# Performance work log

Measured on AMD Instinct MI355X. Metric: run time of the kernel, lower is better.

## Reference

```python
import jax, jax.numpy as jnp
import numpy as np

B, N, D, L = 32, 512, 768, 4  # batch, nodes (incl. CLS at last index), in_dim==hidden_size, num_layers


def setup_inputs() -> dict:
    key = jax.random.key(0)
    ks = jax.random.split(key, 6)
    feature = jax.random.normal(ks[0], (B, N, D), jnp.float32)
    # token mask: random valid lengths, CLS node at the last index always present
    lengths = jax.random.randint(ks[1], (B,), N // 2, N)
    pmask = (jnp.arange(N)[None, :] < lengths[:, None]).astype(jnp.float32)
    pmask = pmask.at[:, -1].set(1.0)
    # L2C (learning-to-connect) bilinear gate params, one pair per layer
    Wq = jax.random.normal(ks[2], (L, D, D), jnp.float32) / np.sqrt(D)
    Wk = jax.random.normal(ks[3], (L, D, D), jnp.float32) / np.sqrt(D)
    # attention-pool projection Linear(in_dim, 1)
    proj_w = jax.random.normal(ks[4], (D,), jnp.float32) / np.sqrt(D)
    proj_b = jnp.zeros((), jnp.float32)
    return dict(pmask=pmask, feature=feature, Wq=Wq, Wk=Wk, proj_w=proj_w, proj_b=proj_b)


def reference(pmask, feature, Wq, Wk, proj_w, proj_b):
    full_adj = pmask[:, :, None] * pmask[:, None, :]        # [B,N,N]
    full_sum = jnp.sum(full_adj) + 1e-8
    p_sum = pmask.sum(-1)                                    # [B]
    scale = 1.0 / np.sqrt(D)
    preds = [feature]
    adjs, c_list, g_list = [], [], []
    total_l0 = jnp.zeros((), feature.dtype)
    for l in range(L):
        # L2C: bilinear sigmoid gate masked by full adjacency, L0-style loss = mean gate mass
        q = jnp.einsum('bnd,de->bne', feature, Wq[l])
        k = jnp.einsum('bnd,de->bne', feature, Wk[l])
        adj = jax.nn.sigmoid(jnp.einsum('bne,bme->bnm', q, k) * scale) * full_adj  # [B,N,N]
        total_l0 = total_l0 + jnp.sum(adj) / full_sum
        # sparse_statistics: CLS-row sparsity and graph-edge sparsity
        c_list.append(adj[:, -1, :-1].sum(-1) / p_sum)               # [B]
        g_list.append(adj[:, :-1, :-1].sum((-1, -2)) / p_sum ** 2)   # [B]
        adjs.append(adj)
        # symmetric degree normalization: D^-1/2 A D^-1/2 (diag bmm == row/col scaling)
        deg = adj.sum(2)                                              # [B,N]
        dis = jnp.where(deg > 0, jax.lax.rsqrt(jnp.maximum(deg, 1e-12)), 0.0)
        dis = jax.lax.stop_gradient(dis)                              # .detach() in original
        adj_n = dis[:, :, None] * adj * dis[:, None, :]
        # feature = adj_^T @ feature
        feature = jnp.einsum('bnm,bnd->bmd', adj_n, feature)
        preds.append(feature)
    pps = jnp.stack(preds, axis=2)                                    # [B,N,L+1,D]
    retain = jax.nn.sigmoid(jnp.einsum('bnld,d->bnl', pps, proj_w) + proj_b)  # [B,N,L+1]
    out = jnp.einsum('bnl,bnld->bnd', retain, pps)                    # [B,N,D]
    c_sparsity = jnp.stack(c_list, axis=-1)                           # [B,L]
    g_sparsity = jnp.stack(g_list, axis=-1)                           # [B,L]
    return (out, retain, jnp.stack(adjs, axis=-1), total_l0 / L, c_sparsity, g_sparsity)
```

## Files before the change

### kernel.cpp

```cpp
#include <hip/hip_runtime.h>

typedef short s16x8 __attribute__((ext_vector_type(8)));
typedef float f32x4 __attribute__((ext_vector_type(4)));

constexpr int BATCH = 32, NODES = 512, DIM = 768, LAYERS = 4;
constexpr float QK_SCALE = 0.03608439182435161f;

constexpr size_t OUT_OFF  = 0;
constexpr size_t RET_OFF  = (size_t)BATCH * NODES * DIM;
constexpr size_t ADJS_OFF = RET_OFF + (size_t)BATCH * NODES * (LAYERS + 1);
constexpr size_t L0_OFF   = ADJS_OFF + (size_t)BATCH * NODES * NODES * LAYERS;
constexpr size_t C_OFF    = L0_OFF + 1;
constexpr size_t G_OFF    = C_OFF + BATCH * LAYERS;

#define DEVI static __device__ __forceinline__

DEVI float bf2f(unsigned short u) {
    union { unsigned int i; float f; } v; v.i = ((unsigned int)u) << 16; return v.f;
}
DEVI unsigned short f2bf(float f) {
    union { float f; unsigned int i; } v; v.f = f;
    return (unsigned short)((v.i + 0x7FFFu + ((v.i >> 16) & 1u)) >> 16);
}
DEVI ushort4 pk4(float4 v) {
    ushort4 o; o.x = f2bf(v.x); o.y = f2bf(v.y); o.z = f2bf(v.z); o.w = f2bf(v.w); return o;
}
DEVI float sigm(float x) { return 1.0f / (1.0f + __expf(-x)); }
DEVI float deg2dis(float d) { return d > 0.f ? rsqrtf(fmaxf(d, 1e-12f)) : 0.f; }

DEVI void gload16(const unsigned short* g, unsigned short* l) {
    __builtin_amdgcn_global_load_lds(
        (const __attribute__((address_space(1))) unsigned int*)g,
        (__attribute__((address_space(3))) unsigned int*)l, 16, 0, 0);
}

template <int MODE>
__global__ __launch_bounds__(512) void gemm256_nt(
    const unsigned short* __restrict__ A0, const unsigned short* __restrict__ B0,
    unsigned short* __restrict__ C0,
    int K, int lda, int ldb, int ldc,
    long sA, long sB, long sC,
    const float* __restrict__ pmask, float* __restrict__ deg,
    unsigned short* __restrict__ adjT,
    float* __restrict__ l0_acc, float* __restrict__ c_acc, float* __restrict__ g_acc,
    int layer)
{
    __shared__ __align__(16) unsigned short lds[2][2][2][8192];
    __shared__ float pmr[256];
    __shared__ float pmc[256];

    const int tid  = threadIdx.x;
    const int lane = tid & 63;
    const int wave = tid >> 6;
    const int wm   = wave >> 2;
    const int wn   = wave & 3;
    const int z = blockIdx.z;
    const int rows0 = blockIdx.x << 8;
    const int cols0 = blockIdx.y << 8;

    const unsigned short* A = A0 + (size_t)z * sA;
    const unsigned short* B = B0 + (size_t)z * sB;

    if constexpr (MODE == 1) {
        if (tid < 256) pmr[tid] = pmask[(size_t)z * NODES + rows0 + tid];
        else pmc[tid - 256] = pmask[(size_t)z * NODES + cols0 + (tid - 256)];
    }

    const int srow  = lane >> 3;
    const int scol8 = (lane & 7) ^ srow;

    auto stage_half = [&](int T, int op, int h) {
        const int base = (op == 0) ? rows0 : cols0;
        const int ld   = (op == 0) ? lda : ldb;
        const unsigned short* src = ((op == 0) ? A : B)
            + (size_t)(base + h * 128 + wave * 8 + srow) * ld + (size_t)T * 64 + scol8 * 8;
        unsigned short* dst = &lds[T & 1][op][h][wave * 512];
        gload16(src, dst);
        gload16(src + (size_t)64 * ld, dst + 4096);
    };

    const int nkt = K >> 6;

    stage_half(0, 0, 0); stage_half(0, 0, 1);
    stage_half(0, 1, 0); stage_half(0, 1, 1);
    if (nkt > 1) {
        stage_half(1, 0, 0);
        asm volatile("s_waitcnt vmcnt(2)" ::: "memory");
    } else {
        asm volatile("s_waitcnt vmcnt(0)" ::: "memory");
    }
    __builtin_amdgcn_s_barrier();
    asm volatile("" ::: "memory");

    f32x4 acc[8][4] = {};

    const int fr = lane & 15;
    const int fq = lane >> 4;
    const int xk = (fr & 7) << 4;
    const int frow64 = fr * 64;
    const int ka0 = ((fq * 16) ^ xk) >> 1;
    const int ka1 = ((64 + fq * 16) ^ xk) >> 1;
    const int brow = (wn & 1) * 4096;

    for (int T = 0; T < nkt; ++T) {
        const unsigned short* Ah = &lds[T & 1][0][wm][0];
        const unsigned short* Bh = &lds[T & 1][1][wn >> 1][0];
        s16x8 af[4][2], bq[4][2];

        #pragma unroll
        for (int i = 0; i < 4; ++i) {
            af[i][0] = *(const s16x8*)(Ah + i * 1024 + frow64 + ka0);
            af[i][1] = *(const s16x8*)(Ah + i * 1024 + frow64 + ka1);
        }
        #pragma unroll
        for (int j = 0; j < 2; ++j) {
            bq[j][0] = *(const s16x8*)(Bh + brow + j * 1024 + frow64 + ka0);
            bq[j][1] = *(const s16x8*)(Bh + brow + j * 1024 + frow64 + ka1);
        }
        if (T + 1 < nkt) stage_half(T + 1, 0, 1);
        asm volatile("" ::: "memory");
        __builtin_amdgcn_s_barrier();
        asm volatile("s_waitcnt lgkmcnt(0)" ::: "memory");
        __builtin_amdgcn_sched_barrier(0);
        __builtin_amdgcn_s_setprio(1);
        #pragma unroll
        for (int i = 0; i < 4; ++i)
            #pragma unroll
            for (int j = 0; j < 2; ++j)
                #pragma unroll
                for (int s = 0; s < 2; ++s)
                    acc[i][j] = __builtin_amdgcn_mfma_f32_16x16x32_bf16(af[i][s], bq[j][s], acc[i][j], 0, 0, 0);
        __builtin_amdgcn_s_setprio(0);
        asm volatile("" ::: "memory");
        __builtin_amdgcn_s_barrier();
        asm volatile("" ::: "memory");

        #pragma unroll
        for (int j = 0; j < 2; ++j) {
            bq[2 + j][0] = *(const s16x8*)(Bh + brow + (2 + j) * 1024 + frow64 + ka0);
            bq[2 + j][1] = *(const s16x8*)(Bh + brow + (2 + j) * 1024 + frow64 + ka1);
        }
        if (T + 1 < nkt) stage_half(T + 1, 1, 0);
        asm volatile("" ::: "memory");
        __builtin_amdgcn_s_barrier();
        asm volatile("s_waitcnt lgkmcnt(0)" ::: "memory");
        __builtin_amdgcn_sched_barrier(0);
        __builtin_amdgcn_s_setprio(1);
        #pragma unroll
        for (int i = 0; i < 4; ++i)
            #pragma unroll
            for (int j = 2; j < 4; ++j)
                #pragma unroll
                for (int s = 0; s < 2; ++s)
                    acc[i][j] = __builtin_amdgcn_mfma_f32_16x16x32_bf16(af[i][s], bq[j][s], acc[i][j], 0, 0, 0);
        __builtin_amdgcn_s_setprio(0);
        asm volatile("" ::: "memory");
        __builtin_amdgcn_s_barrier();
        asm volatile("" ::: "memory");

        #pragma unroll
        for (int i = 0; i < 4; ++i) {
            af[i][0] = *(const s16x8*)(Ah + (4 + i) * 1024 + frow64 + ka0);
            af[i][1] = *(const s16x8*)(Ah + (4 + i) * 1024 + frow64 + ka1);
        }
        if (T + 1 < nkt) stage_half(T + 1, 1, 1);
        asm volatile("" ::: "memory");
        __builtin_amdgcn_s_barrier();
        asm volatile("s_waitcnt lgkmcnt(0)" ::: "memory");
        __builtin_amdgcn_sched_barrier(0);
        __builtin_amdgcn_s_setprio(1);
        #pragma unroll
        for (int i = 0; i < 4; ++i)
            #pragma unroll
            for (int j = 2; j < 4; ++j)
                #pragma unroll
                for (int s = 0; s < 2; ++s)
                    acc[4 + i][j] = __builtin_amdgcn_mfma_f32_16x16x32_bf16(af[i][s], bq[j][s], acc[4 + i][j], 0, 0, 0);
        __builtin_amdgcn_s_setprio(0);
        asm volatile("" ::: "memory");
        __builtin_amdgcn_s_barrier();
        asm volatile("" ::: "memory");

        if (T + 2 < nkt) stage_half(T + 2, 0, 0);
        asm volatile("" ::: "memory");
        __builtin_amdgcn_s_barrier();
        asm volatile("" ::: "memory");
        __builtin_amdgcn_s_setprio(1);
        #pragma unroll
        for (int i = 0; i < 4; ++i)
            #pragma unroll
            for (int j = 0; j < 2; ++j)
                #pragma unroll
                for (int s = 0; s < 2; ++s)
                    acc[4 + i][j] = __builtin_amdgcn_mfma_f32_16x16x32_bf16(af[i][s], bq[j][s], acc[4 + i][j], 0, 0, 0);
        __builtin_amdgcn_s_setprio(0);
        if (T + 2 < nkt) asm volatile("s_waitcnt vmcnt(2)" ::: "memory");
        else             asm volatile("s_waitcnt vmcnt(0)" ::: "memory");
        __builtin_amdgcn_s_barrier();
        asm volatile("" ::: "memory");
    }

    const int quad4 = fq << 2;

    if constexpr (MODE != 1) {
        unsigned short* C = C0 + (size_t)z * sC;
        #pragma unroll
        for (int i = 0; i < 8; ++i) {
            const int rbase = rows0 + wm * 128 + i * 16 + quad4;
            float dv[4];
            if constexpr (MODE == 2) {
                #pragma unroll
                for (int r = 0; r < 4; ++r) dv[r] = deg2dis(deg[(size_t)z * NODES + rbase + r]);
            }
            #pragma unroll
            for (int j = 0; j < 4; ++j) {
                const int cc = cols0 + wn * 64 + j * 16 + fr;
                #pragma unroll
                for (int r = 0; r < 4; ++r) {
                    float v = acc[i][j][r];
                    if constexpr (MODE == 2) v *= dv[r];
                    C[(size_t)(rbase + r) * ldc + cc] = f2bf(v);
                }
            }
        }
    } else {
        float tot = 0.f, gs = 0.f, cs = 0.f;
        #pragma unroll
        for (int i = 0; i < 8; ++i) {
            const int nloc = wm * 128 + i * 16 + quad4;
            #pragma unroll
            for (int r = 0; r < 4; ++r) {
                const int n = rows0 + nloc + r;
                const float pmn = pmr[nloc + r];
                float dp = 0.f;
                #pragma unroll
                for (int j = 0; j < 4; ++j) {
                    const int mloc = wn * 64 + j * 16 + fr;
                    const int m = cols0 + mloc;
                    float a = pmn * pmc[mloc] * sigm(acc[i][j][r] * QK_SCALE);
                    acc[i][j][r] = a;
                    dp += a;
                    tot += a;
                    if (m < NODES - 1) {
                        if (n < NODES - 1) gs += a;
                        else cs += a;
                    }
                }
                dp += __shfl_xor(dp, 1, 16);
                dp += __shfl_xor(dp, 2, 16);
                dp += __shfl_xor(dp, 4, 16);
                dp += __shfl_xor(dp, 8, 16);
                if (fr == 0) atomicAdd(&deg[(size_t)z * NODES + n], dp);
            }
        }
        #pragma unroll
        for (int i = 0; i < 8; ++i) {
            const int nb = rows0 + wm * 128 + i * 16 + quad4;
            #pragma unroll
            for (int j = 0; j < 4; ++j) {
                const int m = cols0 + wn * 64 + j * 16 + fr;
                ushort4 pk;
                pk.x = f2bf(acc[i][j][0]); pk.y = f2bf(acc[i][j][1]);
                pk.z = f2bf(acc[i][j][2]); pk.w = f2bf(acc[i][j][3]);
                *(ushort4*)(adjT + ((size_t)z * NODES + m) * NODES + nb) = pk;
            }
        }
        #pragma unroll
        for (int o = 1; o < 64; o <<= 1) {
            tot += __shfl_xor(tot, o, 64);
            gs  += __shfl_xor(gs, o, 64);
            cs  += __shfl_xor(cs, o, 64);
        }
        if (lane == 0) {
            atomicAdd(l0_acc, tot);
            atomicAdd(&g_acc[z * LAYERS + layer], gs);
            atomicAdd(&c_acc[z * LAYERS + layer], cs);
        }
    }
}

__global__ void fp_transpose(const unsigned short* __restrict__ X, const float* __restrict__ deg,
                             unsigned short* __restrict__ fpt)
{
    __shared__ unsigned short t[32][36];
    const int b = blockIdx.z;
    const int n0 = blockIdx.x << 5, d0 = blockIdx.y << 5;
    const int tr = threadIdx.x >> 3, tc = (threadIdx.x & 7) << 2;
    const float dv = deg2dis(deg[(size_t)b * NODES + n0 + tr]);
    ushort4 v = *(const ushort4*)(X + ((size_t)b * NODES + n0 + tr) * DIM + d0 + tc);
    t[tr][tc]     = f2bf(bf2f(v.x) * dv);
    t[tr][tc + 1] = f2bf(bf2f(v.y) * dv);
    t[tr][tc + 2] = f2bf(bf2f(v.z) * dv);
    t[tr][tc + 3] = f2bf(bf2f(v.w) * dv);
    __syncthreads();
    ushort4 o;
    o.x = t[tc + 0][tr]; o.y = t[tc + 1][tr]; o.z = t[tc + 2][tr]; o.w = t[tc + 3][tr];
    *(ushort4*)(fpt + ((size_t)b * DIM + d0 + tr) * NODES + n0 + tc) = o;
}

DEVI void mt_tile(const float* __restrict__ A, const float* __restrict__ B,
                  unsigned short* __restrict__ C,
                  unsigned short* As, unsigned short* Bs, int rows0, int cols0)
{
    const int tid  = threadIdx.x;
    const int lane = tid & 63;
    const int wave = tid >> 6;
    const int wr = (wave >> 1) << 6;
    const int wc = (wave & 1) << 6;

    const int srow = wave * 16 + (lane >> 2);
    const int scb  = (lane & 3) << 3;
    const float* Ag = A + (size_t)(rows0 + srow) * DIM + scb;
    const float* Bg = B + (size_t)(cols0 + srow) * DIM + scb;
    unsigned short* pa = &As[srow * 32 + scb];
    unsigned short* pb = &Bs[srow * 32 + scb];

    f32x4 acc[4][4] = {};
    const int mrow = lane & 15;
    const int kq   = (lane >> 4) << 3;

    for (int kt = 0; kt < DIM; kt += 32) {
        __syncthreads();
        float4 a0 = *(const float4*)(Ag + kt);
        float4 a1 = *(const float4*)(Ag + kt + 4);
        float4 a2 = *(const float4*)(Ag + (size_t)64 * DIM + kt);
        float4 a3 = *(const float4*)(Ag + (size_t)64 * DIM + kt + 4);
        float4 b0 = *(const float4*)(Bg + kt);
        float4 b1 = *(const float4*)(Bg + kt + 4);
        float4 b2 = *(const float4*)(Bg + (size_t)64 * DIM + kt);
        float4 b3 = *(const float4*)(Bg + (size_t)64 * DIM + kt + 4);
        *(ushort4*)(pa)               = pk4(a0);
        *(ushort4*)(pa + 4)           = pk4(a1);
        *(ushort4*)(pa + 64 * 32)     = pk4(a2);
        *(ushort4*)(pa + 64 * 32 + 4) = pk4(a3);
        *(ushort4*)(pb)               = pk4(b0);
        *(ushort4*)(pb + 4)           = pk4(b1);
        *(ushort4*)(pb + 64 * 32)     = pk4(b2);
        *(ushort4*)(pb + 64 * 32 + 4) = pk4(b3);
        __syncthreads();

        s16x8 af[4], bfr[4];
        #pragma unroll
        for (int i = 0; i < 4; ++i) {
            af[i]  = *(const s16x8*)(&As[(wr + i * 16 + mrow) * 32 + kq]);
            bfr[i] = *(const s16x8*)(&Bs[(wc + i * 16 + mrow) * 32 + kq]);
        }
        #pragma unroll
        for (int i = 0; i < 4; ++i)
            #pragma unroll
            for (int j = 0; j < 4; ++j)
                acc[i][j] = __builtin_amdgcn_mfma_f32_16x16x32_bf16(af[i], bfr[j], acc[i][j], 0, 0, 0);
    }

    const int colb = lane & 15, quad = lane >> 4;
    #pragma unroll
    for (int i = 0; i < 4; ++i) {
        const int rbase = rows0 + wr + i * 16 + (quad << 2);
        #pragma unroll
        for (int j = 0; j < 4; ++j) {
            const int cc = cols0 + wc + j * 16 + colb;
            #pragma unroll
            for (int r = 0; r < 4; ++r)
                C[(size_t)(rbase + r) * DIM + cc] = f2bf(acc[i][j][r]);
        }
    }
}

__global__ __launch_bounds__(256) void cast_all(
    const float* __restrict__ feat, const float* __restrict__ Wq,
    const float* __restrict__ Wk, unsigned short* __restrict__ featb,
    unsigned short* __restrict__ MT,
    const float* __restrict__ pm, float* __restrict__ ps,
    float* __restrict__ zbase)
{
    __shared__ __align__(16) unsigned short As[128 * 32];
    __shared__ __align__(16) unsigned short Bs[128 * 32];
    __shared__ float sh[4];

    const int bx = blockIdx.x;
    if (bx < 12288) {
        const size_t i = (size_t)bx * 1024 + ((size_t)threadIdx.x << 2);
        float4 v = *(const float4*)(feat + i);
        *(ushort4*)(featb + i) = pk4(v);
        return;
    }
    if (bx < 12320) {
        const int b = bx - 12288, t = threadIdx.x;
        float s = pm[(size_t)b * NODES + t] + pm[(size_t)b * NODES + 256 + t];
        #pragma unroll
        for (int o = 1; o < 64; o <<= 1) s += __shfl_xor(s, o, 64);
        if ((t & 63) == 0) sh[t >> 6] = s;
        __syncthreads();
        if (t == 0) ps[b] = sh[0] + sh[1] + sh[2] + sh[3];
        return;
    }
    if (bx < 12385) {
        const int idx = (bx - 12320) * 256 + threadIdx.x;
        if (idx < 16464) ((float4*)zbase)[idx] = float4{0.f, 0.f, 0.f, 0.f};
        return;
    }
    const int r = bx - 12385;
    const int z = r / 36, rem = r % 36;
    mt_tile(Wk + (size_t)z * DIM * DIM, Wq + (size_t)z * DIM * DIM,
            MT + (size_t)z * DIM * DIM, As, Bs,
            (rem / 6) << 7, (rem % 6) << 7);
}

__global__ __launch_bounds__(256) void tail_out(
    const unsigned short* __restrict__ adjT,
    const float* __restrict__ X0f, const unsigned short* __restrict__ X1,
    const unsigned short* __restrict__ X2, const unsigned short* __restrict__ X3,
    const unsigned short* __restrict__ X4,
    const float* __restrict__ pw, const float* __restrict__ pb,
    const float* __restrict__ ps, const float* __restrict__ c_acc,
    const float* __restrict__ g_acc, const float* __restrict__ l0,
    float* __restrict__ ob)
{
    const int bid = blockIdx.x;
    if (bid < 8192) {
        __shared__ unsigned short t[4][32][36];
        float* adjs = ob + ADJS_OFF;
        const int b = bid >> 8, m0 = (bid & 15) << 5, n0 = ((bid >> 4) & 15) << 5;
        const int tr = threadIdx.x >> 3, tc = (threadIdx.x & 7) << 2;
        #pragma unroll
        for (int l = 0; l < LAYERS; ++l) {
            ushort4 v = *(const ushort4*)(adjT + (((size_t)l * BATCH + b) * NODES + m0 + tr) * NODES + n0 + tc);
            t[l][tr][tc] = v.x; t[l][tr][tc + 1] = v.y; t[l][tr][tc + 2] = v.z; t[l][tr][tc + 3] = v.w;
        }
        __syncthreads();
        float* dst = adjs + (((size_t)b * NODES + n0 + tr) * NODES + m0 + tc) * LAYERS;
        #pragma unroll
        for (int mm = 0; mm < 4; ++mm) {
            float4 f;
            f.x = bf2f(t[0][tc + mm][tr]); f.y = bf2f(t[1][tc + mm][tr]);
            f.z = bf2f(t[2][tc + mm][tr]); f.w = bf2f(t[3][tc + mm][tr]);
            *(float4*)(dst + mm * 4) = f;
        }
        return;
    }

    const int fb = bid - 8192;
    if (fb == 0) {
        const int t = threadIdx.x;
        if (t < BATCH * LAYERS) {
            const int b = t >> 2;
            const float p = ps[b];
            ob[C_OFF + t] = c_acc[t] / p;
            ob[G_OFF + t] = g_acc[t] / (p * p);
        }
        if (t == 0) {
            float fs = 1e-8f;
            for (int b = 0; b < BATCH; ++b) fs += ps[b] * ps[b];
            ob[L0_OFF] = l0[0] / (fs * (float)LAYERS);
        }
    }

    const int row = (fb << 2) + (threadIdx.x >> 6);
    const int lane = threadIdx.x & 63;
    const unsigned short* Xb[4] = { X1 + (size_t)row * DIM, X2 + (size_t)row * DIM,
                                    X3 + (size_t)row * DIM, X4 + (size_t)row * DIM };
    float xs[5][12];
    float dot[5] = {};
    #pragma unroll
    for (int c = 0; c < 3; ++c) {
        const int idx = c * 256 + (lane << 2);
        float4 wv = *(const float4*)(pw + idx);
        float4 x0 = *(const float4*)(X0f + (size_t)row * DIM + idx);
        xs[0][c * 4 + 0] = x0.x; xs[0][c * 4 + 1] = x0.y;
        xs[0][c * 4 + 2] = x0.z; xs[0][c * 4 + 3] = x0.w;
        dot[0] += x0.x * wv.x + x0.y * wv.y + x0.z * wv.z + x0.w * wv.w;
        #pragma unroll
        for (int l = 0; l < 4; ++l) {
            ushort4 xv = *(const ushort4*)(Xb[l] + idx);
            float a0 = bf2f(xv.x), a1 = bf2f(xv.y), a2 = bf2f(xv.z), a3 = bf2f(xv.w);
            xs[l + 1][c * 4 + 0] = a0; xs[l + 1][c * 4 + 1] = a1;
            xs[l + 1][c * 4 + 2] = a2; xs[l + 1][c * 4 + 3] = a3;
            dot[l + 1] += a0 * wv.x + a1 * wv.y + a2 * wv.z + a3 * wv.w;
        }
    }
    #pragma unroll
    for (int l = 0; l < 5; ++l)
        #pragma unroll
        for (int o = 1; o < 64; o <<= 1) dot[l] += __shfl_xor(dot[l], o, 64);
    const float pbv = pb[0];
    float r[5];
    #pragma unroll
    for (int l = 0; l < 5; ++l) r[l] = sigm(dot[l] + pbv);
    if (lane == 0) {
        float* rr = ob + RET_OFF + (size_t)row * (LAYERS + 1);
        rr[0] = r[0]; rr[1] = r[1]; rr[2] = r[2]; rr[3] = r[3]; rr[4] = r[4];
    }
    float* orow = ob + OUT_OFF + (size_t)row * DIM;
    #pragma unroll
    for (int c = 0; c < 3; ++c) {
        float4 p;
        p.x = r[0] * xs[0][c * 4 + 0]; p.y = r[0] * xs[0][c * 4 + 1];
        p.z = r[0] * xs[0][c * 4 + 2]; p.w = r[0] * xs[0][c * 4 + 3];
        #pragma unroll
        for (int l = 1; l < 5; ++l) {
            p.x += r[l] * xs[l][c * 4 + 0]; p.y += r[l] * xs[l][c * 4 + 1];
            p.z += r[l] * xs[l][c * 4 + 2]; p.w += r[l] * xs[l][c * 4 + 3];
        }
        *(float4*)(orow + c * 256 + (lane << 2)) = p;
    }
}

extern "C" void kernel_launch(void* const* d_in, const int* in_sizes, int n_in,
                              void* d_out, int out_size, void* d_ws, size_t ws_size,
                              hipStream_t stream)
{
    (void)in_sizes; (void)n_in; (void)out_size; (void)ws_size;
    const float* pmask = (const float*)d_in[0];
    const float* feat  = (const float*)d_in[1];
    const float* Wq    = (const float*)d_in[2];
    const float* Wk    = (const float*)d_in[3];
    const float* projw = (const float*)d_in[4];
    const float* projb = (const float*)d_in[5];
    float* ob = (float*)d_out;

    char* w = (char*)d_ws;
    unsigned short* Xb[4];
    Xb[0] = (unsigned short*)(w + 0);
    Xb[1] = (unsigned short*)(w + 25165824);
    Xb[2] = (unsigned short*)(w + 50331648);
    Xb[3] = (unsigned short*)(w + 75497472);
    unsigned short* qws   = (unsigned short*)(w + 100663296);
    unsigned short* featb = (unsigned short*)(w + 125829120);
    unsigned short* adjT  = (unsigned short*)(w + 150994944);
    unsigned short* MT    = (unsigned short*)(w + 227540992);
    float* deg_all = (float*)(w + 232259584);
    float* c_acc   = (float*)(w + 232521728);
    float* g_acc   = (float*)(w + 232522240);
    float* l0_acc  = (float*)(w + 232522752);
    float* p_sum   = (float*)(w + 232523008);

    dim3 blk(256);
    dim3 blk5(512);

    cast_all<<<dim3(12529), blk, 0, stream>>>(feat, Wq, Wk, featb, MT,
                                              pmask, p_sum, deg_all);

    for (int l = 0; l < LAYERS; ++l) {
        float* deg_l = deg_all + (size_t)l * BATCH * NODES;
        unsigned short* adjT_l = adjT + (size_t)l * BATCH * NODES * NODES;
        const unsigned short* Xsrc = (l == 0) ? featb : Xb[l - 1];

        gemm256_nt<0><<<dim3(64, 3, 1), blk5, 0, stream>>>(
            Xsrc, MT + (size_t)l * DIM * DIM, qws,
            DIM, DIM, DIM, DIM, 0L, 0L, 0L,
            nullptr, nullptr, nullptr, nullptr, nullptr, nullptr, 0);

        gemm256_nt<1><<<dim3(2, 2, 32), blk5, 0, stream>>>(
            qws, Xsrc, nullptr,
            DIM, DIM, DIM, 0, (long)NODES * DIM, (long)NODES * DIM, 0L,
            pmask, deg_l, adjT_l, l0_acc, c_acc, g_acc, l);

        fp_transpose<<<dim3(16, 24, 32), blk, 0, stream>>>(Xsrc, deg_l, qws);

        gemm256_nt<2><<<dim3(2, 3, 32), blk5, 0, stream>>>(
            adjT_l, qws, Xb[l],
            NODES, NODES, NODES, DIM, (long)NODES * NODES, (long)DIM * NODES, (long)NODES * DIM,
            nullptr, deg_l, nullptr, nullptr, nullptr, nullptr, 0);
    }

    tail_out<<<dim3(12288), blk, 0, stream>>>(adjT, feat, Xb[0], Xb[1], Xb[2], Xb[3],
                                              projw, projb, p_sum, c_acc, g_acc, l0_acc, ob);
}
```

Measured before the change: 789.3 us.

## Shrink GEMM tiles from 256x256 with 8 waves to 128x128 with 4 waves

Replaces the 256x256 tile, 512-thread GEMM with a 128x128 tile, 256-thread version and rewrites the LDS staging and the per-iteration MFMA schedule to match. Grids grow fourfold (for example 192 to 768 blocks for the projection GEMM and 128 to 512 for the batched ones). This gives better occupancy and load balance across the CUs, which 128–192 blocks underfill. The cost is less operand reuse per tile, so global and LDS traffic per FLOP rises.

```diff
diff --git a/kernel.cpp b/kernel.cpp
--- a/kernel.cpp
+++ b/kernel.cpp
@@ -35,7 +35,7 @@
 }
 
 template <int MODE>
-__global__ __launch_bounds__(512) void gemm256_nt(
+__global__ __launch_bounds__(256) void gemm128_nt(
     const unsigned short* __restrict__ A0, const unsigned short* __restrict__ B0,
     unsigned short* __restrict__ C0,
     int K, int lda, int ldb, int ldc,
@@ -45,54 +45,55 @@
     float* __restrict__ l0_acc, float* __restrict__ c_acc, float* __restrict__ g_acc,
     int layer)
 {
-    __shared__ __align__(16) unsigned short lds[2][2][2][8192];
-    __shared__ float pmr[256];
-    __shared__ float pmc[256];
+    __shared__ __align__(16) unsigned short lds[2][2][8192];
+    __shared__ float pmr[128];
+    __shared__ float pmc[128];
 
     const int tid  = threadIdx.x;
     const int lane = tid & 63;
     const int wave = tid >> 6;
-    const int wm   = wave >> 2;
-    const int wn   = wave & 3;
+    const int wm   = wave >> 1;
+    const int wn   = wave & 1;
     const int z = blockIdx.z;
-    const int rows0 = blockIdx.x << 8;
-    const int cols0 = blockIdx.y << 8;
+    const int rows0 = blockIdx.x << 7;
+    const int cols0 = blockIdx.y << 7;
 
     const unsigned short* A = A0 + (size_t)z * sA;
     const unsigned short* B = B0 + (size_t)z * sB;
 
     if constexpr (MODE == 1) {
-        if (tid < 256) pmr[tid] = pmask[(size_t)z * NODES + rows0 + tid];
-        else pmc[tid - 256] = pmask[(size_t)z * NODES + cols0 + (tid - 256)];
+        if (tid < 128) pmr[tid] = pmask[(size_t)z * NODES + rows0 + tid];
+        else pmc[tid - 128] = pmask[(size_t)z * NODES + cols0 + (tid - 128)];
     }
 
     const int srow  = lane >> 3;
     const int scol8 = (lane & 7) ^ srow;
 
-    auto stage_half = [&](int T, int op, int h) {
-        const int base = (op == 0) ? rows0 : cols0;
-        const int ld   = (op == 0) ? lda : ldb;
-        const unsigned short* src = ((op == 0) ? A : B)
-            + (size_t)(base + h * 128 + wave * 8 + srow) * ld + (size_t)T * 64 + scol8 * 8;
-        unsigned short* dst = &lds[T & 1][op][h][wave * 512];
-        gload16(src, dst);
-        gload16(src + (size_t)64 * ld, dst + 4096);
+    auto stage = [&](int T, int op) {
+        const int base = op ? cols0 : rows0;
+        const int ld   = op ? ldb : lda;
+        const unsigned short* srcb = op ? B : A;
+        #pragma unroll
+        for (int g = 0; g < 4; ++g) {
+            const unsigned short* src = srcb
+                + (size_t)(base + g * 32 + wave * 8 + srow) * ld + (size_t)T * 64 + scol8 * 8;
+            gload16(src, &lds[T & 1][op][g * 2048 + wave * 512]);
+        }
     };
 
     const int nkt = K >> 6;
 
-    stage_half(0, 0, 0); stage_half(0, 0, 1);
-    stage_half(0, 1, 0); stage_half(0, 1, 1);
+    stage(0, 0); stage(0, 1);
     if (nkt > 1) {
-        stage_half(1, 0, 0);
-        asm volatile("s_waitcnt vmcnt(2)" ::: "memory");
+        stage(1, 0);
+        asm volatile("s_waitcnt vmcnt(4)" ::: "memory");
     } else {
         asm volatile("s_waitcnt vmcnt(0)" ::: "memory");
     }
     __builtin_amdgcn_s_barrier();
     asm volatile("" ::: "memory");
 
-    f32x4 acc[8][4] = {};
+    f32x4 acc[4][4] = {};
 
     const int fr = lane & 15;
     const int fq = lane >> 4;
@@ -100,11 +101,10 @@
     const int frow64 = fr * 64;
     const int ka0 = ((fq * 16) ^ xk) >> 1;
     const int ka1 = ((64 + fq * 16) ^ xk) >> 1;
-    const int brow = (wn & 1) * 4096;
 
     for (int T = 0; T < nkt; ++T) {
-        const unsigned short* Ah = &lds[T & 1][0][wm][0];
-        const unsigned short* Bh = &lds[T & 1][1][wn >> 1][0];
+        const unsigned short* Ah = &lds[T & 1][0][wm * 4096];
+        const unsigned short* Bh = &lds[T & 1][1][wn * 4096];
         s16x8 af[4][2], bq[4][2];
 
         #pragma unroll
@@ -114,10 +114,10 @@
         }
         #pragma unroll
         for (int j = 0; j < 2; ++j) {
-            bq[j][0] = *(const s16x8*)(Bh + brow + j * 1024 + frow64 + ka0);
-            bq[j][1] = *(const s16x8*)(Bh + brow + j * 1024 + frow64 + ka1);
-        }
-        if (T + 1 < nkt) stage_half(T + 1, 0, 1);
+            bq[j][0] = *(const s16x8*)(Bh + j * 1024 + frow64 + ka0);
+            bq[j][1] = *(const s16x8*)(Bh + j * 1024 + frow64 + ka1);
+        }
+        if (T + 1 < nkt) stage(T + 1, 1);
         asm volatile("" ::: "memory");
         __builtin_amdgcn_s_barrier();
         asm volatile("s_waitcnt lgkmcnt(0)" ::: "memory");
@@ -136,11 +136,11 @@
         asm volatile("" ::: "memory");
 
         #pragma unroll
-        for (int j = 0; j < 2; ++j) {
-            bq[2 + j][0] = *(const s16x8*)(Bh + brow + (2 + j) * 1024 + frow64 + ka0);
-            bq[2 + j][1] = *(const s16x8*)(Bh + brow + (2 + j) * 1024 + frow64 + ka1);
-        }
-        if (T + 1 < nkt) stage_half(T + 1, 1, 0);
+        for (int j = 2; j < 4; ++j) {
+            bq[j][0] = *(const s16x8*)(Bh + j * 1024 + frow64 + ka0);
+            bq[j][1] = *(const s16x8*)(Bh + j * 1024 + frow64 + ka1);
+        }
+        if (T + 2 < nkt) stage(T + 2, 0);
         asm volatile("" ::: "memory");
         __builtin_amdgcn_s_barrier();
         asm volatile("s_waitcnt lgkmcnt(0)" ::: "memory");
@@ -154,47 +154,7 @@
                 for (int s = 0; s < 2; ++s)
                     acc[i][j] = __builtin_amdgcn_mfma_f32_16x16x32_bf16(af[i][s], bq[j][s], acc[i][j], 0, 0, 0);
         __builtin_amdgcn_s_setprio(0);
-        asm volatile("" ::: "memory");
-        __builtin_amdgcn_s_barrier();
-        asm volatile("" ::: "memory");
-
-        #pragma unroll
-        for (int i = 0; i < 4; ++i) {
-            af[i][0] = *(const s16x8*)(Ah + (4 + i) * 1024 + frow64 + ka0);
-            af[i][1] = *(const s16x8*)(Ah + (4 + i) * 1024 + frow64 + ka1);
-        }
-        if (T + 1 < nkt) stage_half(T + 1, 1, 1);
-        asm volatile("" ::: "memory");
-        __builtin_amdgcn_s_barrier();
-        asm volatile("s_waitcnt lgkmcnt(0)" ::: "memory");
-        __builtin_amdgcn_sched_barrier(0);
-        __builtin_amdgcn_s_setprio(1);
-        #pragma unroll
-        for (int i = 0; i < 4; ++i)
-            #pragma unroll
-            for (int j = 2; j < 4; ++j)
-                #pragma unroll
-                for (int s = 0; s < 2; ++s)
-                    acc[4 + i][j] = __builtin_amdgcn_mfma_f32_16x16x32_bf16(af[i][s], bq[j][s], acc[4 + i][j], 0, 0, 0);
-        __builtin_amdgcn_s_setprio(0);
-        asm volatile("" ::: "memory");
-        __builtin_amdgcn_s_barrier();
-        asm volatile("" ::: "memory");
-
-        if (T + 2 < nkt) stage_half(T + 2, 0, 0);
-        asm volatile("" ::: "memory");
-        __builtin_amdgcn_s_barrier();
-        asm volatile("" ::: "memory");
-        __builtin_amdgcn_s_setprio(1);
-        #pragma unroll
-        for (int i = 0; i < 4; ++i)
-            #pragma unroll
-            for (int j = 0; j < 2; ++j)
-                #pragma unroll
-                for (int s = 0; s < 2; ++s)
-                    acc[4 + i][j] = __builtin_amdgcn_mfma_f32_16x16x32_bf16(af[i][s], bq[j][s], acc[4 + i][j], 0, 0, 0);
-        __builtin_amdgcn_s_setprio(0);
-        if (T + 2 < nkt) asm volatile("s_waitcnt vmcnt(2)" ::: "memory");
+        if (T + 2 < nkt) asm volatile("s_waitcnt vmcnt(4)" ::: "memory");
         else             asm volatile("s_waitcnt vmcnt(0)" ::: "memory");
         __builtin_amdgcn_s_barrier();
         asm volatile("" ::: "memory");
@@ -205,8 +165,8 @@
     if constexpr (MODE != 1) {
         unsigned short* C = C0 + (size_t)z * sC;
         #pragma unroll
-        for (int i = 0; i < 8; ++i) {
-            const int rbase = rows0 + wm * 128 + i * 16 + quad4;
+        for (int i = 0; i < 4; ++i) {
+            const int rbase = rows0 + wm * 64 + i * 16 + quad4;
             float dv[4];
             if constexpr (MODE == 2) {
                 #pragma unroll
@@ -226,8 +186,8 @@
     } else {
         float tot = 0.f, gs = 0.f, cs = 0.f;
         #pragma unroll
-        for (int i = 0; i < 8; ++i) {
-            const int nloc = wm * 128 + i * 16 + quad4;
+        for (int i = 0; i < 4; ++i) {
+            const int nloc = wm * 64 + i * 16 + quad4;
             #pragma unroll
             for (int r = 0; r < 4; ++r) {
                 const int n = rows0 + nloc + r;
@@ -254,8 +214,8 @@
             }
         }
         #pragma unroll
-        for (int i = 0; i < 8; ++i) {
-            const int nb = rows0 + wm * 128 + i * 16 + quad4;
+        for (int i = 0; i < 4; ++i) {
+            const int nb = rows0 + wm * 64 + i * 16 + quad4;
             #pragma unroll
             for (int j = 0; j < 4; ++j) {
                 const int m = cols0 + wn * 64 + j * 16 + fr;
@@ -535,7 +495,6 @@
     float* p_sum   = (float*)(w + 232523008);
 
     dim3 blk(256);
-    dim3 blk5(512);
 
     cast_all<<<dim3(12529), blk, 0, stream>>>(feat, Wq, Wk, featb, MT,
                                               pmask, p_sum, deg_all);
@@ -545,19 +504,19 @@
         unsigned short* adjT_l = adjT + (size_t)l * BATCH * NODES * NODES;
         const unsigned short* Xsrc = (l == 0) ? featb : Xb[l - 1];
 
-        gemm256_nt<0><<<dim3(64, 3, 1), blk5, 0, stream>>>(
+        gemm128_nt<0><<<dim3(128, 6, 1), blk, 0, stream>>>(
             Xsrc, MT + (size_t)l * DIM * DIM, qws,
             DIM, DIM, DIM, DIM, 0L, 0L, 0L,
             nullptr, nullptr, nullptr, nullptr, nullptr, nullptr, 0);
 
-        gemm256_nt<1><<<dim3(2, 2, 32), blk5, 0, stream>>>(
+        gemm128_nt<1><<<dim3(4, 4, 32), blk, 0, stream>>>(
             qws, Xsrc, nullptr,
             DIM, DIM, DIM, 0, (long)NODES * DIM, (long)NODES * DIM, 0L,
             pmask, deg_l, adjT_l, l0_acc, c_acc, g_acc, l);
 
         fp_transpose<<<dim3(16, 24, 32), blk, 0, stream>>>(Xsrc, deg_l, qws);
 
-        gemm256_nt<2><<<dim3(2, 3, 32), blk5, 0, stream>>>(
+        gemm128_nt<2><<<dim3(4, 6, 32), blk, 0, stream>>>(
             adjT_l, qws, Xb[l],
             NODES, NODES, NODES, DIM, (long)NODES * NODES, (long)DIM * NODES, (long)NODES * DIM,
             nullptr, deg_l, nullptr, nullptr, nullptr, nullptr, 0);
```

New measurement: 798.6 us. Within noise of the previous version (+1.2%).
